# Kernel optimization log

Hardware: AMD Instinct MI355X
Metric: run time of the kernel (lower is better)

The kernel has to match this reference:

```python
import jax, jax.numpy as jnp
import numpy as np

H = 256  # hidden_size
T = 4096  # sequence length
IN = 128  # input_size


def _lstm_dir(x_seq, Wih, Whh, b, reverse):
    # x_seq: [T, D_in]; Wih: [4H, D_in]; Whh: [4H, H]; b: [4H]
    xs = x_seq @ Wih.T + b  # precompute input projection [T, 4H]
    if reverse:
        xs = xs[::-1]

    def step(carry, xt):
        h, c = carry
        z = xt + h @ Whh.T
        i, f, g, o = jnp.split(z, 4, axis=-1)  # torch gate order i,f,g,o
        c = jax.nn.sigmoid(f) * c + jax.nn.sigmoid(i) * jnp.tanh(g)
        h = jax.nn.sigmoid(o) * jnp.tanh(c)
        return (h, c), h

    init = (jnp.zeros((H,), x_seq.dtype), jnp.zeros((H,), x_seq.dtype))
    _, hs = jax.lax.scan(step, init, xs)
    if reverse:
        hs = hs[::-1]
    return hs  # [T, H]


def _bilstm_layer(x_seq, Wih_f, Whh_f, b_f, Wih_b, Whh_b, b_b):
    hf = _lstm_dir(x_seq, Wih_f, Whh_f, b_f, False)
    hb = _lstm_dir(x_seq, Wih_b, Whh_b, b_b, True)
    return jnp.concatenate([hf, hb], axis=-1)  # [T, 2H]


def setup_inputs() -> dict:
    key = jax.random.key(0)
    ks = jax.random.split(key, 20)
    s = 1.0 / np.sqrt(H)

    def g(k, shape):
        return (jax.random.normal(k, shape, dtype=jnp.float32) * s)

    inp = {
        "x": jax.random.normal(ks[0], (1, T, IN), dtype=jnp.float32),
        # layer 0 (input dim IN), fwd / bwd directions; b = b_ih + b_hh folded
        "wih_l0f": g(ks[1], (4 * H, IN)), "whh_l0f": g(ks[2], (4 * H, H)), "b_l0f": g(ks[3], (4 * H,)),
        "wih_l0b": g(ks[4], (4 * H, IN)), "whh_l0b": g(ks[5], (4 * H, H)), "b_l0b": g(ks[6], (4 * H,)),
        # layer 1 (input dim 2H)
        "wih_l1f": g(ks[7], (4 * H, 2 * H)), "whh_l1f": g(ks[8], (4 * H, H)), "b_l1f": g(ks[9], (4 * H,)),
        "wih_l1b": g(ks[10], (4 * H, 2 * H)), "whh_l1b": g(ks[11], (4 * H, H)), "b_l1b": g(ks[12], (4 * H,)),
        # fc1: Linear(512, 256); fc2: Linear(256, 256)
        "fc1_w": g(ks[13], (256, 512)), "fc1_b": g(ks[14], (256,)),
        "fc2_w": g(ks[15], (256, 256)), "fc2_b": g(ks[16], (256,)),
    }
    return inp


def reference(x, wih_l0f, whh_l0f, b_l0f, wih_l0b, whh_l0b, b_l0b,
              wih_l1f, whh_l1f, b_l1f, wih_l1b, whh_l1b, b_l1b,
              fc1_w, fc1_b, fc2_w, fc2_b):
    xs = x[0]  # squeeze batch of 1 -> [T, IN]
    h1 = _bilstm_layer(xs, wih_l0f, whh_l0f, b_l0f, wih_l0b, whh_l0b, b_l0b)  # [T, 512]
    h2 = _bilstm_layer(h1, wih_l1f, whh_l1f, b_l1f, wih_l1b, whh_l1b, b_l1b)  # [T, 512]
    z = jnp.maximum(h2 @ fc1_w.T + fc1_b, 0.0)  # ReLU(fc1)
    e = z @ fc2_w.T + fc2_b  # [T, 256]
    # fused pairwise cosine similarity (replaces the per-row python loop)
    norms = jnp.linalg.norm(e, axis=1)  # [T]
    cs = (e @ e.T) / (norms[:, None] * norms[None, :])
    cs = jnp.maximum(cs, 1e-6)  # torch.clamp(min=1e-6)
    return 1.0 - cs  # [T, T]
```

## Files before the change

### kernel.cpp

```cpp
#include <hip/hip_runtime.h>
#include <hip/hip_fp16.h>

#define T_LEN 4096
#define HID   256
#define G4    1024
#define DIRSZ (1024 * 128)

typedef unsigned int u32;
typedef unsigned long long u64;
typedef _Float16 half2_t __attribute__((ext_vector_type(2)));

__device__ __forceinline__ float dot2f(u32 w, u32 h, float acc) {
#if __has_builtin(__builtin_amdgcn_fdot2)
    return __builtin_amdgcn_fdot2(__builtin_bit_cast(half2_t, w),
                                  __builtin_bit_cast(half2_t, h), acc, false);
#else
    __half2 wh = __builtin_bit_cast(__half2, w);
    __half2 hh = __builtin_bit_cast(__half2, h);
    float2 wf = __half22float2(wh), hf = __half22float2(hh);
    return acc + wf.x * hf.x + wf.y * hf.y;
#endif
}

__device__ __forceinline__ float qsum(float v) {
    int i = __builtin_bit_cast(int, v);
    v += __builtin_bit_cast(float,
         __builtin_amdgcn_update_dpp(i, i, 0xB1, 0xF, 0xF, true));
    i = __builtin_bit_cast(int, v);
    v += __builtin_bit_cast(float,
         __builtin_amdgcn_update_dpp(i, i, 0x4E, 0xF, 0xF, true));
    return v;
}

__device__ __forceinline__ u32 pack2(float a, float b) {
    unsigned short lo = __half_as_ushort(__float2half(a));
    unsigned short hi = __half_as_ushort(__float2half(b));
    return ((u32)hi << 16) | (u32)lo;
}

__device__ __forceinline__ void step_barrier() {
    asm volatile("s_waitcnt lgkmcnt(0)" ::: "memory");
    __builtin_amdgcn_s_barrier();
    __builtin_amdgcn_sched_barrier(0);
}

__global__ void k_zero(u32* __restrict__ p, int n) {
    int q = blockIdx.x * 256 + threadIdx.x;
    if (q < n) p[q] = 0u;
}

__global__ void k_transpose(const float* __restrict__ in, float* __restrict__ out,
                            int N, int K) {
    int q = blockIdx.x * 256 + threadIdx.x;
    if (q >= N * K) return;
    int n = q / K, k = q % K;
    out[(size_t)k * N + n] = in[q];
}

__global__ void k_pack_q4(const float* __restrict__ W, u32* __restrict__ out) {
    int idx = blockIdx.x * 256 + threadIdx.x;
    if (idx >= 1024 * 128) return;
    int widx = idx & 127;
    int tid  = (idx >> 7) & 511;
    int sl   = idx >> 16;
    int g = widx >> 5, rem = widx & 31;
    int bb = rem >> 2, i = rem & 3;
    int j = tid >> 2, qq = tid & 3;
    int row = g * 256 + 128 * sl + j;
    int pair = 32 * qq + 4 * ((bb + 2 * qq) & 7) + i;
    out[idx] = pack2(W[row * 256 + 2 * pair], W[row * 256 + 2 * pair + 1]);
}

__global__ __launch_bounds__(256) void k_gemm(
    const float* __restrict__ A, const float* __restrict__ Wt,
    const float* __restrict__ bias, const float* __restrict__ norms,
    float* __restrict__ C, int M, int N, int K, int mode) {
    __shared__ float As[16 * 512];
    const int tid = threadIdx.x;
    const int m0 = blockIdx.x * 16;
    const int n  = blockIdx.y * 256 + tid;

    for (int i = tid; i < 16 * K; i += 256) As[i] = A[(size_t)m0 * K + i];
    __syncthreads();

    float acc[16];
#pragma unroll
    for (int m = 0; m < 16; ++m) acc[m] = 0.f;

#pragma unroll 4
    for (int k = 0; k < K; ++k) {
        float w = Wt[(size_t)k * N + n];
#pragma unroll
        for (int m = 0; m < 16; ++m) acc[m] += As[m * K + k] * w;
    }

    float bn = bias ? bias[n] : 0.f;
#pragma unroll
    for (int m = 0; m < 16; ++m) {
        float v = acc[m] + bn;
        if (mode == 1) v = fmaxf(v, 0.f);
        if (mode == 2) {
            float d = norms[m0 + m] * norms[n];
            v = 1.f - fmaxf(acc[m] / d, 1e-6f);
        }
        C[(size_t)(m0 + m) * N + n] = v;
    }
}

__global__ void k_norms(const float* __restrict__ e, float* __restrict__ norms) {
    int i = blockIdx.x, lane = threadIdx.x;
    float s = 0.f;
    for (int k = lane; k < 256; k += 64) { float v = e[i * 256 + k]; s += v * v; }
    for (int off = 32; off; off >>= 1) s += __shfl_down(s, off);
    if (lane == 0) norms[i] = sqrtf(s);
}

__global__ __launch_bounds__(512, 2) void k_scan_q4(
    const float* __restrict__ xs, const u32* __restrict__ rp,
    u64* __restrict__ ex, float* __restrict__ hout) {
    __shared__ alignas(16) u32 hb[2][128];

    const int bid = blockIdx.x;
    if ((bid & 7) > 1 || (bid >> 3) > 1) return;
    const int dir = bid & 7;
    const int s   = bid >> 3;
    const int rs  = 1 - s;
    const int tid = threadIdx.x;
    const int j   = tid >> 2;
    const int q   = tid & 3;
    const int U   = 128 * s + j;

    xs += (size_t)dir * (T_LEN * G4);
    rp += (size_t)dir * DIRSZ;
    u64* exd = ex + dir * (2 * 2 * 64);

    u32 regw[128];
    {
        const uint4* rp4 = (const uint4*)(rp + (size_t)(s * 512 + tid) * 128);
#pragma unroll
        for (int p = 0; p < 32; ++p) {
            uint4 v = rp4[p];
            regw[4 * p + 0] = v.x; regw[4 * p + 1] = v.y;
            regw[4 * p + 2] = v.z; regw[4 * p + 3] = v.w;
        }
    }
    if (tid < 128) { hb[0][tid] = 0u; hb[1][tid] = 0u; }
    float cst = 0.f;
    __syncthreads();

    int tt = dir ? (T_LEN - 1) : 0;
    const int stp = dir ? -1 : 1;
    float xa = xs[(size_t)tt * G4 + (q * 256 + U)];

    for (int t = 0; t < T_LEN; ++t) {
        const int cur = t & 1, nxt = cur ^ 1;
        int tn = (t + 1 < T_LEN) ? tt + stp : tt;
        float acc0 = (q == 0) ? xa : 0.f;
        float acc1 = (q == 1) ? xa : 0.f;
        float acc2 = (q == 2) ? xa : 0.f;
        float acc3 = (q == 3) ? xa : 0.f;
        xa = xs[(size_t)tn * G4 + (q * 256 + U)];

        const u32* hq = &hb[cur][32 * q];
#pragma unroll
        for (int bb = 0; bb < 8; ++bb) {
            uint4 hv4 = *(const uint4*)&hq[4 * ((bb + 2 * q) & 7)];
            u32 hh[4] = { hv4.x, hv4.y, hv4.z, hv4.w };
#pragma unroll
            for (int i = 0; i < 4; ++i) {
                const int p = 4 * bb + i;
                acc0 = dot2f(regw[p],       hh[i], acc0);
                acc1 = dot2f(regw[32 + p],  hh[i], acc1);
                acc2 = dot2f(regw[64 + p],  hh[i], acc2);
                acc3 = dot2f(regw[96 + p],  hh[i], acc3);
            }
        }

        float zi = qsum(acc0), zf = qsum(acc1), zg = qsum(acc2), zo = qsum(acc3);

        float si = 1.f / (1.f + __expf(-zi));
        float sf = 1.f / (1.f + __expf(-zf));
        float so = 1.f / (1.f + __expf(-zo));
        float tg = 1.f - 2.f / (__expf(2.f * zg) + 1.f);
        cst = sf * cst + si * tg;
        float th = 1.f - 2.f / (__expf(2.f * cst) + 1.f);
        float hv = so * th;

        float hn = __shfl_xor(hv, 4);

        if (q == 0)
            ((__half*)hb[nxt])[128 * s + j] = __float2half(hv);
        if (q == 0 && !(j & 1)) {
            u32 hp = pack2(hv, hn);
            u64 pay = ((u64)(u32)(t + 1) << 32) | (u64)hp;
            __hip_atomic_store(&exd[(cur * 2 + s) * 64 + (j >> 1)], pay,
                               __ATOMIC_RELAXED, __HIP_MEMORY_SCOPE_AGENT);
        }
        if (q == 1)
            hout[(size_t)tt * 512 + dir * 256 + U] = hv;
        if (q == 3 && (j & 1) && (t + 1 < T_LEN)) {
            u64 v;
            do {
                v = __hip_atomic_load(&exd[(cur * 2 + rs) * 64 + (j >> 1)],
                                      __ATOMIC_RELAXED, __HIP_MEMORY_SCOPE_AGENT);
            } while ((u32)(v >> 32) != (u32)(t + 1));
            hb[nxt][64 * rs + (j >> 1)] = (u32)v;
        }
        step_barrier();
        tt = tn;
    }
}

extern "C" void kernel_launch(void* const* d_in, const int* in_sizes, int n_in,
                              void* d_out, int out_size, void* d_ws, size_t ws_size,
                              hipStream_t stream) {
    const float* x       = (const float*)d_in[0];
    const float* wih_l0f = (const float*)d_in[1];
    const float* whh_l0f = (const float*)d_in[2];
    const float* b_l0f   = (const float*)d_in[3];
    const float* wih_l0b = (const float*)d_in[4];
    const float* whh_l0b = (const float*)d_in[5];
    const float* b_l0b   = (const float*)d_in[6];
    const float* wih_l1f = (const float*)d_in[7];
    const float* whh_l1f = (const float*)d_in[8];
    const float* b_l1f   = (const float*)d_in[9];
    const float* wih_l1b = (const float*)d_in[10];
    const float* whh_l1b = (const float*)d_in[11];
    const float* b_l1b   = (const float*)d_in[12];
    const float* fc1_w   = (const float*)d_in[13];
    const float* fc1_b   = (const float*)d_in[14];
    const float* fc2_w   = (const float*)d_in[15];
    const float* fc2_b   = (const float*)d_in[16];
    float* outp = (float*)d_out;

    char* ws = (char*)d_ws;
    size_t off = 0;
    auto alloc = [&](size_t nbytes) {
        char* p = ws + off;
        off += (nbytes + 255) & ~(size_t)255;
        return p;
    };
    float* xs0   = (float*)alloc((size_t)2 * T_LEN * G4 * 4);
    float* xs1   = (float*)alloc((size_t)2 * T_LEN * G4 * 4);
    float* h1    = (float*)alloc((size_t)T_LEN * 512 * 4);
    float* h2    = (float*)alloc((size_t)T_LEN * 512 * 4);
    float* zb    = (float*)alloc((size_t)T_LEN * 256 * 4);
    float* eb    = (float*)alloc((size_t)T_LEN * 256 * 4);
    float* etb   = (float*)alloc((size_t)T_LEN * 256 * 4);
    float* nrm   = (float*)alloc((size_t)T_LEN * 4);
    float* wt0f  = (float*)alloc((size_t)128 * 1024 * 4);
    float* wt0b  = (float*)alloc((size_t)128 * 1024 * 4);
    float* wt1f  = (float*)alloc((size_t)512 * 1024 * 4);
    float* wt1b  = (float*)alloc((size_t)512 * 1024 * 4);
    float* wtf1  = (float*)alloc((size_t)512 * 256 * 4);
    float* wtf2  = (float*)alloc((size_t)256 * 256 * 4);
    u32*   rpm0  = (u32*)alloc((size_t)2 * DIRSZ * 4);
    u32*   rpm1  = (u32*)alloc((size_t)2 * DIRSZ * 4);
    u64*   exA   = (u64*)alloc((size_t)512 * 8);
    u64*   exB   = (u64*)alloc((size_t)512 * 8);

    k_zero<<<8, 256, 0, stream>>>((u32*)exA, 2048);

    k_transpose<<<(1024 * 128 + 255) / 256, 256, 0, stream>>>(wih_l0f, wt0f, 1024, 128);
    k_transpose<<<(1024 * 128 + 255) / 256, 256, 0, stream>>>(wih_l0b, wt0b, 1024, 128);
    k_transpose<<<(1024 * 512 + 255) / 256, 256, 0, stream>>>(wih_l1f, wt1f, 1024, 512);
    k_transpose<<<(1024 * 512 + 255) / 256, 256, 0, stream>>>(wih_l1b, wt1b, 1024, 512);
    k_transpose<<<(256 * 512 + 255) / 256, 256, 0, stream>>>(fc1_w, wtf1, 256, 512);
    k_transpose<<<(256 * 256 + 255) / 256, 256, 0, stream>>>(fc2_w, wtf2, 256, 256);

    k_pack_q4<<<512, 256, 0, stream>>>(whh_l0f, rpm0);
    k_pack_q4<<<512, 256, 0, stream>>>(whh_l0b, rpm0 + DIRSZ);
    k_pack_q4<<<512, 256, 0, stream>>>(whh_l1f, rpm1);
    k_pack_q4<<<512, 256, 0, stream>>>(whh_l1b, rpm1 + DIRSZ);

    dim3 g1024(T_LEN / 16, 4);
    k_gemm<<<g1024, 256, 0, stream>>>(x, wt0f, b_l0f, nullptr, xs0, T_LEN, 1024, 128, 0);
    k_gemm<<<g1024, 256, 0, stream>>>(x, wt0b, b_l0b, nullptr, xs0 + (size_t)T_LEN * G4, T_LEN, 1024, 128, 0);
    k_scan_q4<<<16, 512, 0, stream>>>(xs0, rpm0, exA, h1);
    k_gemm<<<g1024, 256, 0, stream>>>(h1, wt1f, b_l1f, nullptr, xs1, T_LEN, 1024, 512, 0);
    k_gemm<<<g1024, 256, 0, stream>>>(h1, wt1b, b_l1b, nullptr, xs1 + (size_t)T_LEN * G4, T_LEN, 1024, 512, 0);
    k_scan_q4<<<16, 512, 0, stream>>>(xs1, rpm1, exB, h2);
    k_gemm<<<dim3(T_LEN / 16, 1), 256, 0, stream>>>(h2, wtf1, fc1_b, nullptr, zb, T_LEN, 256, 512, 1);
    k_gemm<<<dim3(T_LEN / 16, 1), 256, 0, stream>>>(zb, wtf2, fc2_b, nullptr, eb, T_LEN, 256, 256, 0);
    k_transpose<<<(T_LEN * 256 + 255) / 256, 256, 0, stream>>>(eb, etb, T_LEN, 256);
    k_norms<<<T_LEN, 64, 0, stream>>>(eb, nrm);
    k_gemm<<<dim3(T_LEN / 16, T_LEN / 256), 256, 0, stream>>>(eb, etb, nullptr, nrm, outp, T_LEN, T_LEN, 256, 2);
}
```

Before: 12.52 ms.

## Split each LSTM direction's recurrence across four blocks instead of two

```diff
diff --git a/kernel.cpp b/kernel.cpp
--- a/kernel.cpp
+++ b/kernel.cpp
@@ -22,13 +22,15 @@
 #endif
 }
 
-__device__ __forceinline__ float qsum(float v) {
+__device__ __forceinline__ float qsum8(float v) {
     int i = __builtin_bit_cast(int, v);
     v += __builtin_bit_cast(float,
          __builtin_amdgcn_update_dpp(i, i, 0xB1, 0xF, 0xF, true));
     i = __builtin_bit_cast(int, v);
     v += __builtin_bit_cast(float,
          __builtin_amdgcn_update_dpp(i, i, 0x4E, 0xF, 0xF, true));
+    i = __builtin_bit_cast(int, v);
+    v += __builtin_bit_cast(float, __builtin_amdgcn_ds_swizzle(i, 0x101F));
     return v;
 }
 
@@ -57,17 +59,17 @@
     out[(size_t)k * N + n] = in[q];
 }
 
-__global__ void k_pack_q4(const float* __restrict__ W, u32* __restrict__ out) {
+__global__ void k_pack_q8(const float* __restrict__ W, u32* __restrict__ out) {
     int idx = blockIdx.x * 256 + threadIdx.x;
     if (idx >= 1024 * 128) return;
-    int widx = idx & 127;
-    int tid  = (idx >> 7) & 511;
-    int sl   = idx >> 16;
-    int g = widx >> 5, rem = widx & 31;
+    int widx = idx & 63;
+    int tid  = (idx >> 6) & 511;
+    int sl   = idx >> 15;
+    int g = widx >> 4, rem = widx & 15;
     int bb = rem >> 2, i = rem & 3;
-    int j = tid >> 2, qq = tid & 3;
-    int row = g * 256 + 128 * sl + j;
-    int pair = 32 * qq + 4 * ((bb + 2 * qq) & 7) + i;
+    int j = tid >> 3, q = tid & 7;
+    int row = g * 256 + 64 * sl + j;
+    int pair = 16 * q + 4 * ((bb + q) & 3) + i;
     out[idx] = pack2(W[row * 256 + 2 * pair], W[row * 256 + 2 * pair + 1]);
 }
 
@@ -115,30 +117,29 @@
     if (lane == 0) norms[i] = sqrtf(s);
 }
 
-__global__ __launch_bounds__(512, 2) void k_scan_q4(
+__global__ __launch_bounds__(512, 2) void k_scan_q8(
     const float* __restrict__ xs, const u32* __restrict__ rp,
     u64* __restrict__ ex, float* __restrict__ hout) {
     __shared__ alignas(16) u32 hb[2][128];
 
     const int bid = blockIdx.x;
-    if ((bid & 7) > 1 || (bid >> 3) > 1) return;
-    const int dir = bid & 7;
-    const int s   = bid >> 3;
-    const int rs  = 1 - s;
+    const int dir = bid & 1;
+    const int s   = bid >> 1;
     const int tid = threadIdx.x;
-    const int j   = tid >> 2;
-    const int q   = tid & 3;
-    const int U   = 128 * s + j;
+    const int j   = tid >> 3;
+    const int q   = tid & 7;
+    const int gq  = q & 3;
+    const int U   = 64 * s + j;
 
     xs += (size_t)dir * (T_LEN * G4);
     rp += (size_t)dir * DIRSZ;
-    u64* exd = ex + dir * (2 * 2 * 64);
-
-    u32 regw[128];
+    u64* exd = ex + dir * 256;
+
+    u32 regw[64];
     {
-        const uint4* rp4 = (const uint4*)(rp + (size_t)(s * 512 + tid) * 128);
-#pragma unroll
-        for (int p = 0; p < 32; ++p) {
+        const uint4* rp4 = (const uint4*)(rp + (size_t)(s * 512 + tid) * 64);
+#pragma unroll
+        for (int p = 0; p < 16; ++p) {
             uint4 v = rp4[p];
             regw[4 * p + 0] = v.x; regw[4 * p + 1] = v.y;
             regw[4 * p + 2] = v.z; regw[4 * p + 3] = v.w;
@@ -150,7 +151,7 @@
 
     int tt = dir ? (T_LEN - 1) : 0;
     const int stp = dir ? -1 : 1;
-    float xa = xs[(size_t)tt * G4 + (q * 256 + U)];
+    float xa = xs[(size_t)tt * G4 + (gq * 256 + U)];
 
     for (int t = 0; t < T_LEN; ++t) {
         const int cur = t & 1, nxt = cur ^ 1;
@@ -159,24 +160,25 @@
         float acc1 = (q == 1) ? xa : 0.f;
         float acc2 = (q == 2) ? xa : 0.f;
         float acc3 = (q == 3) ? xa : 0.f;
-        xa = xs[(size_t)tn * G4 + (q * 256 + U)];
-
-        const u32* hq = &hb[cur][32 * q];
-#pragma unroll
-        for (int bb = 0; bb < 8; ++bb) {
-            uint4 hv4 = *(const uint4*)&hq[4 * ((bb + 2 * q) & 7)];
+        xa = xs[(size_t)tn * G4 + (gq * 256 + U)];
+
+        const u32* hq = &hb[cur][16 * q];
+#pragma unroll
+        for (int bb = 0; bb < 4; ++bb) {
+            uint4 hv4 = *(const uint4*)&hq[4 * ((bb + q) & 3)];
             u32 hh[4] = { hv4.x, hv4.y, hv4.z, hv4.w };
 #pragma unroll
             for (int i = 0; i < 4; ++i) {
                 const int p = 4 * bb + i;
                 acc0 = dot2f(regw[p],       hh[i], acc0);
-                acc1 = dot2f(regw[32 + p],  hh[i], acc1);
-                acc2 = dot2f(regw[64 + p],  hh[i], acc2);
-                acc3 = dot2f(regw[96 + p],  hh[i], acc3);
+                acc1 = dot2f(regw[16 + p],  hh[i], acc1);
+                acc2 = dot2f(regw[32 + p],  hh[i], acc2);
+                acc3 = dot2f(regw[48 + p],  hh[i], acc3);
             }
         }
 
-        float zi = qsum(acc0), zf = qsum(acc1), zg = qsum(acc2), zo = qsum(acc3);
+        float zi = qsum8(acc0), zf = qsum8(acc1);
+        float zg = qsum8(acc2), zo = qsum8(acc3);
 
         float si = 1.f / (1.f + __expf(-zi));
         float sf = 1.f / (1.f + __expf(-zf));
@@ -186,25 +188,28 @@
         float th = 1.f - 2.f / (__expf(2.f * cst) + 1.f);
         float hv = so * th;
 
-        float hn = __shfl_xor(hv, 4);
+        float hn = __builtin_bit_cast(float,
+            __builtin_amdgcn_ds_swizzle(__builtin_bit_cast(int, hv), 0x201F));
 
         if (q == 0)
-            ((__half*)hb[nxt])[128 * s + j] = __float2half(hv);
+            ((__half*)hb[nxt])[64 * s + j] = __float2half(hv);
         if (q == 0 && !(j & 1)) {
             u32 hp = pack2(hv, hn);
             u64 pay = ((u64)(u32)(t + 1) << 32) | (u64)hp;
-            __hip_atomic_store(&exd[(cur * 2 + s) * 64 + (j >> 1)], pay,
+            __hip_atomic_store(&exd[(cur * 4 + s) * 32 + (j >> 1)], pay,
                                __ATOMIC_RELAXED, __HIP_MEMORY_SCOPE_AGENT);
         }
         if (q == 1)
             hout[(size_t)tt * 512 + dir * 256 + U] = hv;
-        if (q == 3 && (j & 1) && (t + 1 < T_LEN)) {
+        if (tid < 96 && (t + 1 < T_LEN)) {
+            int p_ = tid >> 5, w = tid & 31;
+            int ps = (p_ < s) ? p_ : p_ + 1;
             u64 v;
             do {
-                v = __hip_atomic_load(&exd[(cur * 2 + rs) * 64 + (j >> 1)],
+                v = __hip_atomic_load(&exd[(cur * 4 + ps) * 32 + w],
                                       __ATOMIC_RELAXED, __HIP_MEMORY_SCOPE_AGENT);
             } while ((u32)(v >> 32) != (u32)(t + 1));
-            hb[nxt][64 * rs + (j >> 1)] = (u32)v;
+            hb[nxt][32 * ps + w] = (u32)v;
         }
         step_barrier();
         tt = tn;
@@ -268,18 +273,18 @@
     k_transpose<<<(256 * 512 + 255) / 256, 256, 0, stream>>>(fc1_w, wtf1, 256, 512);
     k_transpose<<<(256 * 256 + 255) / 256, 256, 0, stream>>>(fc2_w, wtf2, 256, 256);
 
-    k_pack_q4<<<512, 256, 0, stream>>>(whh_l0f, rpm0);
-    k_pack_q4<<<512, 256, 0, stream>>>(whh_l0b, rpm0 + DIRSZ);
-    k_pack_q4<<<512, 256, 0, stream>>>(whh_l1f, rpm1);
-    k_pack_q4<<<512, 256, 0, stream>>>(whh_l1b, rpm1 + DIRSZ);
+    k_pack_q8<<<512, 256, 0, stream>>>(whh_l0f, rpm0);
+    k_pack_q8<<<512, 256, 0, stream>>>(whh_l0b, rpm0 + DIRSZ);
+    k_pack_q8<<<512, 256, 0, stream>>>(whh_l1f, rpm1);
+    k_pack_q8<<<512, 256, 0, stream>>>(whh_l1b, rpm1 + DIRSZ);
 
     dim3 g1024(T_LEN / 16, 4);
     k_gemm<<<g1024, 256, 0, stream>>>(x, wt0f, b_l0f, nullptr, xs0, T_LEN, 1024, 128, 0);
     k_gemm<<<g1024, 256, 0, stream>>>(x, wt0b, b_l0b, nullptr, xs0 + (size_t)T_LEN * G4, T_LEN, 1024, 128, 0);
-    k_scan_q4<<<16, 512, 0, stream>>>(xs0, rpm0, exA, h1);
+    k_scan_q8<<<8, 512, 0, stream>>>(xs0, rpm0, exA, h1);
     k_gemm<<<g1024, 256, 0, stream>>>(h1, wt1f, b_l1f, nullptr, xs1, T_LEN, 1024, 512, 0);
     k_gemm<<<g1024, 256, 0, stream>>>(h1, wt1b, b_l1b, nullptr, xs1 + (size_t)T_LEN * G4, T_LEN, 1024, 512, 0);
-    k_scan_q4<<<16, 512, 0, stream>>>(xs1, rpm1, exB, h2);
+    k_scan_q8<<<8, 512, 0, stream>>>(xs1, rpm1, exB, h2);
     k_gemm<<<dim3(T_LEN / 16, 1), 256, 0, stream>>>(h2, wtf1, fc1_b, nullptr, zb, T_LEN, 256, 512, 1);
     k_gemm<<<dim3(T_LEN / 16, 1), 256, 0, stream>>>(zb, wtf2, fc2_b, nullptr, eb, T_LEN, 256, 256, 0);
     k_transpose<<<(T_LEN * 256 + 255) / 256, 256, 0, stream>>>(eb, etb, T_LEN, 256);
```

After: 13.54 ms. 1.08x slower.

## Overlap cross-block hidden-state exchange with the local half of the recurrent matvec

Applied to the files above, without the earlier changes.

```diff
diff --git a/kernel.cpp b/kernel.cpp
--- a/kernel.cpp
+++ b/kernel.cpp
@@ -57,17 +57,19 @@
     out[(size_t)k * N + n] = in[q];
 }
 
-__global__ void k_pack_q4(const float* __restrict__ W, u32* __restrict__ out) {
+__global__ void k_pack_sp(const float* __restrict__ W, u32* __restrict__ out) {
     int idx = blockIdx.x * 256 + threadIdx.x;
     if (idx >= 1024 * 128) return;
     int widx = idx & 127;
     int tid  = (idx >> 7) & 511;
     int sl   = idx >> 16;
-    int g = widx >> 5, rem = widx & 31;
-    int bb = rem >> 2, i = rem & 3;
-    int j = tid >> 2, qq = tid & 3;
-    int row = g * 256 + 128 * sl + j;
-    int pair = 32 * qq + 4 * ((bb + 2 * qq) & 7) + i;
+    int g = widx >> 5, half = (widx >> 4) & 1;
+    int bb = (widx >> 2) & 3, i = widx & 3;
+    int j = tid >> 2, q = tid & 3;
+    int U = 128 * sl + j;
+    int row = g * 256 + U;
+    int srcsl = half ? (1 - sl) : sl;
+    int pair = 64 * srcsl + 16 * q + 4 * ((bb + q) & 3) + i;
     out[idx] = pack2(W[row * 256 + 2 * pair], W[row * 256 + 2 * pair + 1]);
 }
 
@@ -115,9 +117,9 @@
     if (lane == 0) norms[i] = sqrtf(s);
 }
 
-__global__ __launch_bounds__(512, 2) void k_scan_q4(
+__global__ __launch_bounds__(512, 2) void k_scan_sp(
     const float* __restrict__ xs, const u32* __restrict__ rp,
-    u64* __restrict__ ex, float* __restrict__ hout) {
+    u32* __restrict__ ex, float* __restrict__ hout) {
     __shared__ alignas(16) u32 hb[2][128];
 
     const int bid = blockIdx.x;
@@ -132,7 +134,7 @@
 
     xs += (size_t)dir * (T_LEN * G4);
     rp += (size_t)dir * DIRSZ;
-    u64* exd = ex + dir * (2 * 2 * 64);
+    u32* exd = ex + dir * 512;
 
     u32 regw[128];
     {
@@ -155,16 +157,22 @@
     for (int t = 0; t < T_LEN; ++t) {
         const int cur = t & 1, nxt = cur ^ 1;
         int tn = (t + 1 < T_LEN) ? tt + stp : tt;
+
+        u32 pv = 0;
+        if (t > 0 && tid < 128)
+            pv = __hip_atomic_load(&exd[cur * 256 + rs * 128 + tid],
+                                   __ATOMIC_RELAXED, __HIP_MEMORY_SCOPE_AGENT);
+
         float acc0 = (q == 0) ? xa : 0.f;
         float acc1 = (q == 1) ? xa : 0.f;
         float acc2 = (q == 2) ? xa : 0.f;
         float acc3 = (q == 3) ? xa : 0.f;
         xa = xs[(size_t)tn * G4 + (q * 256 + U)];
 
-        const u32* hq = &hb[cur][32 * q];
-#pragma unroll
-        for (int bb = 0; bb < 8; ++bb) {
-            uint4 hv4 = *(const uint4*)&hq[4 * ((bb + 2 * q) & 7)];
+        const u32* ho = &hb[cur][64 * s + 16 * q];
+#pragma unroll
+        for (int bb = 0; bb < 4; ++bb) {
+            uint4 hv4 = *(const uint4*)&ho[4 * ((bb + q) & 3)];
             u32 hh[4] = { hv4.x, hv4.y, hv4.z, hv4.w };
 #pragma unroll
             for (int i = 0; i < 4; ++i) {
@@ -176,6 +184,30 @@
             }
         }
 
+        if (t > 0 && tid < 128) {
+            while ((pv >> 16) != (u32)t)
+                pv = __hip_atomic_load(&exd[cur * 256 + rs * 128 + tid],
+                                       __ATOMIC_RELAXED, __HIP_MEMORY_SCOPE_AGENT);
+            ((__half*)hb[cur])[128 * rs + tid] =
+                __ushort_as_half((unsigned short)(pv & 0xffffu));
+        }
+        step_barrier();
+
+        const u32* hr = &hb[cur][64 * rs + 16 * q];
+#pragma unroll
+        for (int bb = 0; bb < 4; ++bb) {
+            uint4 hv4 = *(const uint4*)&hr[4 * ((bb + q) & 3)];
+            u32 hh[4] = { hv4.x, hv4.y, hv4.z, hv4.w };
+#pragma unroll
+            for (int i = 0; i < 4; ++i) {
+                const int p = 16 + 4 * bb + i;
+                acc0 = dot2f(regw[p],       hh[i], acc0);
+                acc1 = dot2f(regw[32 + p],  hh[i], acc1);
+                acc2 = dot2f(regw[64 + p],  hh[i], acc2);
+                acc3 = dot2f(regw[96 + p],  hh[i], acc3);
+            }
+        }
+
         float zi = qsum(acc0), zf = qsum(acc1), zg = qsum(acc2), zo = qsum(acc3);
 
         float si = 1.f / (1.f + __expf(-zi));
@@ -186,26 +218,16 @@
         float th = 1.f - 2.f / (__expf(2.f * cst) + 1.f);
         float hv = so * th;
 
-        float hn = __shfl_xor(hv, 4);
-
-        if (q == 0)
-            ((__half*)hb[nxt])[128 * s + j] = __float2half(hv);
-        if (q == 0 && !(j & 1)) {
-            u32 hp = pack2(hv, hn);
-            u64 pay = ((u64)(u32)(t + 1) << 32) | (u64)hp;
-            __hip_atomic_store(&exd[(cur * 2 + s) * 64 + (j >> 1)], pay,
+        if (q == 0) {
+            unsigned short h16 = __half_as_ushort(__float2half(hv));
+            ((__half*)hb[nxt])[128 * s + j] = __ushort_as_half(h16);
+            __hip_atomic_store(&exd[nxt * 256 + s * 128 + j],
+                               ((u32)(t + 1) << 16) | (u32)h16,
                                __ATOMIC_RELAXED, __HIP_MEMORY_SCOPE_AGENT);
         }
         if (q == 1)
             hout[(size_t)tt * 512 + dir * 256 + U] = hv;
-        if (q == 3 && (j & 1) && (t + 1 < T_LEN)) {
-            u64 v;
-            do {
-                v = __hip_atomic_load(&exd[(cur * 2 + rs) * 64 + (j >> 1)],
-                                      __ATOMIC_RELAXED, __HIP_MEMORY_SCOPE_AGENT);
-            } while ((u32)(v >> 32) != (u32)(t + 1));
-            hb[nxt][64 * rs + (j >> 1)] = (u32)v;
-        }
+
         step_barrier();
         tt = tn;
     }
@@ -256,10 +278,10 @@
     float* wtf2  = (float*)alloc((size_t)256 * 256 * 4);
     u32*   rpm0  = (u32*)alloc((size_t)2 * DIRSZ * 4);
     u32*   rpm1  = (u32*)alloc((size_t)2 * DIRSZ * 4);
-    u64*   exA   = (u64*)alloc((size_t)512 * 8);
-    u64*   exB   = (u64*)alloc((size_t)512 * 8);
-
-    k_zero<<<8, 256, 0, stream>>>((u32*)exA, 2048);
+    u32*   exA   = (u32*)alloc((size_t)1024 * 4);
+    u32*   exB   = (u32*)alloc((size_t)1024 * 4);
+
+    k_zero<<<8, 256, 0, stream>>>(exA, 2048);
 
     k_transpose<<<(1024 * 128 + 255) / 256, 256, 0, stream>>>(wih_l0f, wt0f, 1024, 128);
     k_transpose<<<(1024 * 128 + 255) / 256, 256, 0, stream>>>(wih_l0b, wt0b, 1024, 128);
@@ -268,18 +290,18 @@
     k_transpose<<<(256 * 512 + 255) / 256, 256, 0, stream>>>(fc1_w, wtf1, 256, 512);
     k_transpose<<<(256 * 256 + 255) / 256, 256, 0, stream>>>(fc2_w, wtf2, 256, 256);
 
-    k_pack_q4<<<512, 256, 0, stream>>>(whh_l0f, rpm0);
-    k_pack_q4<<<512, 256, 0, stream>>>(whh_l0b, rpm0 + DIRSZ);
-    k_pack_q4<<<512, 256, 0, stream>>>(whh_l1f, rpm1);
-    k_pack_q4<<<512, 256, 0, stream>>>(whh_l1b, rpm1 + DIRSZ);
+    k_pack_sp<<<512, 256, 0, stream>>>(whh_l0f, rpm0);
+    k_pack_sp<<<512, 256, 0, stream>>>(whh_l0b, rpm0 + DIRSZ);
+    k_pack_sp<<<512, 256, 0, stream>>>(whh_l1f, rpm1);
+    k_pack_sp<<<512, 256, 0, stream>>>(whh_l1b, rpm1 + DIRSZ);
 
     dim3 g1024(T_LEN / 16, 4);
     k_gemm<<<g1024, 256, 0, stream>>>(x, wt0f, b_l0f, nullptr, xs0, T_LEN, 1024, 128, 0);
     k_gemm<<<g1024, 256, 0, stream>>>(x, wt0b, b_l0b, nullptr, xs0 + (size_t)T_LEN * G4, T_LEN, 1024, 128, 0);
-    k_scan_q4<<<16, 512, 0, stream>>>(xs0, rpm0, exA, h1);
+    k_scan_sp<<<16, 512, 0, stream>>>(xs0, rpm0, exA, h1);
     k_gemm<<<g1024, 256, 0, stream>>>(h1, wt1f, b_l1f, nullptr, xs1, T_LEN, 1024, 512, 0);
     k_gemm<<<g1024, 256, 0, stream>>>(h1, wt1b, b_l1b, nullptr, xs1 + (size_t)T_LEN * G4, T_LEN, 1024, 512, 0);
-    k_scan_q4<<<16, 512, 0, stream>>>(xs1, rpm1, exB, h2);
+    k_scan_sp<<<16, 512, 0, stream>>>(xs1, rpm1, exB, h2);
     k_gemm<<<dim3(T_LEN / 16, 1), 256, 0, stream>>>(h2, wtf1, fc1_b, nullptr, zb, T_LEN, 256, 512, 1);
     k_gemm<<<dim3(T_LEN / 16, 1), 256, 0, stream>>>(zb, wtf2, fc2_b, nullptr, eb, T_LEN, 256, 256, 0);
     k_transpose<<<(T_LEN * 256 + 255) / 256, 256, 0, stream>>>(eb, etb, T_LEN, 256);
```

Result: faster. 12.22 ms (-2.4%).
